# Optimization experiments

Hardware: AMD Instinct MI355X
Metric: run time of the kernel (lower is better)

Reference implementation:

```python
import jax, jax.numpy as jnp
import numpy as np

N = 50000          # nodes
E = 800000         # edges (avg degree 16)
IN = 128           # input feature dim
HID = 64           # hidden dim per head
HEADS = 2          # attention heads (all but last layer)
OUT = 64           # out_dim (last layer, 1 head)
NC = 2             # num_classes
NEG_SLOPE = 0.2    # dgl GATConv leaky_relu slope


def setup_inputs() -> dict:
    key = jax.random.key(0)
    ks = jax.random.split(key, 20)
    rn = lambda k, shape, s=0.05: (jax.random.normal(k, shape, jnp.float32) * s)
    W_IO = HID * HEADS  # 128, width between GAT layers
    return {
        "x": rn(ks[0], (N, IN), 1.0),
        "src": jax.random.randint(ks[1], (E,), 0, N, dtype=jnp.int32),
        "dst": jax.random.randint(ks[2], (E,), 0, N, dtype=jnp.int32),
        # embedding_h: Linear(IN, HID*HEADS)
        "W_emb": rn(ks[3], (IN, W_IO)),
        "b_emb": jnp.zeros((W_IO,), jnp.float32),
        # GAT layer 0: in 128 -> 2 heads x 64
        "W0": rn(ks[4], (W_IO, HEADS * HID)),
        "al0": rn(ks[5], (HEADS, HID)),
        "ar0": rn(ks[6], (HEADS, HID)),
        "b0": jnp.zeros((HEADS * HID,), jnp.float32),
        # GAT layer 1: in 128 -> 2 heads x 64
        "W1": rn(ks[7], (W_IO, HEADS * HID)),
        "al1": rn(ks[8], (HEADS, HID)),
        "ar1": rn(ks[9], (HEADS, HID)),
        "b1": jnp.zeros((HEADS * HID,), jnp.float32),
        # GAT layer 2 (last): in 128 -> 1 head x OUT
        "W2": rn(ks[10], (W_IO, 1 * OUT)),
        "al2": rn(ks[11], (1, OUT)),
        "ar2": rn(ks[12], (1, OUT)),
        "b2": jnp.zeros((OUT,), jnp.float32),
        # edge scorer: Linear(2*OUT, NC)
        "Ws": rn(ks[13], (2 * OUT, NC)),
        "bs": jnp.zeros((NC,), jnp.float32),
    }


def gat_layer(h, src, dst, W, al, ar, b):
    """dgl GATConv + elu (GATLayer with batch_norm=False, residual=False)."""
    heads, out = al.shape
    feat = (h @ W).reshape(-1, heads, out)            # [N,H,D]
    el = jnp.sum(feat * al, axis=-1)                  # [N,H]
    er = jnp.sum(feat * ar, axis=-1)                  # [N,H]
    e = jax.nn.leaky_relu(el[src] + er[dst], NEG_SLOPE)  # [E,H]
    # edge softmax over incoming edges of each dst node
    emax = jax.ops.segment_max(e, dst, num_segments=N)   # [N,H]
    ex = jnp.exp(e - emax[dst])                          # [E,H]
    denom = jax.ops.segment_sum(ex, dst, num_segments=N) # [N,H]
    alpha = ex / jnp.where(denom[dst] > 0, denom[dst], 1.0)
    msg = feat[src] * alpha[:, :, None]                  # [E,H,D]
    rst = jax.ops.segment_sum(msg, dst, num_segments=N)  # [N,H,D]
    rst = rst.reshape(-1, heads * out) + b
    return jax.nn.elu(rst)


def reference(x, W_emb, b_emb, W0, al0, ar0, b0, W1, al1, ar1, b1,
              W2, al2, ar2, b2, Ws, bs, src, dst):
    h = x @ W_emb + b_emb                    # embedding_h (dropout p -> eval/identity)
    h = gat_layer(h, src, dst, W0, al0, ar0, b0)
    h = gat_layer(h, src, dst, W1, al1, ar1, b1)
    h = gat_layer(h, src, dst, W2, al2, ar2, b2)   # [N, OUT]
    # edge scorer on the scored subgraph: concat(src_h, dst_h) -> Linear
    he = jnp.concatenate([h[src], h[dst]], axis=1)  # [E, 2*OUT]
    return he @ Ws + bs                             # [E, NC]
```

## Files before the change

kernel.cpp:

```cpp
#include <hip/hip_runtime.h>
#include <hip/hip_bf16.h>
#include <math.h>


constexpr float SLOPE = 0.2f;

typedef __attribute__((ext_vector_type(8))) short bf16x8;
typedef __attribute__((ext_vector_type(4))) float f32x4;

__device__ __forceinline__ float b2f(unsigned short u) {
  union { unsigned int i; float f; } v;
  v.i = ((unsigned int)u) << 16;
  return v.f;
}
__device__ __forceinline__ unsigned short f2b(float f) {
  unsigned int x = __float_as_uint(f);
  unsigned int r = (x + 0x7fffu + ((x >> 16) & 1u)) >> 16;
  return (unsigned short)r;
}

__global__ void prep_wt(const float* __restrict__ W,
                        unsigned short* __restrict__ Wt, int M) {
  int i = blockIdx.x * 256 + threadIdx.x;
  if (i < 128 * M) {
    int k = i / M, m = i - k * M;
    Wt[m * 128 + k] = f2b(W[i]);
  }
}

template<int M, bool AF32>
__global__ __launch_bounds__(256)
void gemm_mfma(const void* __restrict__ Xv,
               const unsigned short* __restrict__ Wt,
               const float* __restrict__ bias,
               const float* __restrict__ al, const float* __restrict__ ar,
               unsigned short* __restrict__ Yb,
               float* __restrict__ el, float* __restrict__ er, int N) {
  constexpr int NT = M / 16;
  constexpr int H = M / 64;

  const int tid = threadIdx.x;
  const int wave = tid >> 6;
  const int lane = tid & 63;
  const int r = lane & 15;
  const int kg = lane >> 4;
  const int rowbase = blockIdx.x * 64 + wave * 16;
  int grow = rowbase + r;
  int growc = grow < N ? grow : N - 1;

  f32x4 acc[NT];
  #pragma unroll
  for (int t = 0; t < NT; ++t) acc[t] = (f32x4){0.f, 0.f, 0.f, 0.f};

  #pragma unroll
  for (int kk = 0; kk < 4; ++kk) {
    const int k0 = kk * 32 + kg * 8;
    bf16x8 a;
    if constexpr (AF32) {
      const float* X = (const float*)Xv;
      const float4* xp =
          reinterpret_cast<const float4*>(X + (size_t)growc * 128 + k0);
      float4 x0 = xp[0], x1 = xp[1];
      a[0] = (short)f2b(x0.x); a[1] = (short)f2b(x0.y);
      a[2] = (short)f2b(x0.z); a[3] = (short)f2b(x0.w);
      a[4] = (short)f2b(x1.x); a[5] = (short)f2b(x1.y);
      a[6] = (short)f2b(x1.z); a[7] = (short)f2b(x1.w);
    } else {
      const unsigned short* Xb = (const unsigned short*)Xv;
      a = *reinterpret_cast<const bf16x8*>(Xb + (size_t)growc * 128 + k0);
    }
    #pragma unroll
    for (int t = 0; t < NT; ++t) {
      bf16x8 b = *reinterpret_cast<const bf16x8*>(
          Wt + (size_t)(t * 16 + r) * 128 + k0);
      acc[t] = __builtin_amdgcn_mfma_f32_16x16x32_bf16(a, b, acc[t], 0, 0, 0);
    }
  }

  float bv[NT];
  #pragma unroll
  for (int t = 0; t < NT; ++t) bv[t] = bias ? bias[t * 16 + r] : 0.f;
  float alv[NT], arv[NT];
  if (al != nullptr) {
    #pragma unroll
    for (int t = 0; t < NT; ++t) {
      alv[t] = al[t * 16 + r];
      arv[t] = ar[t * 16 + r];
    }
  }

  #pragma unroll
  for (int j = 0; j < 4; ++j) {
    int orow = rowbase + kg * 4 + j;
    bool ok = orow < N;
    if (ok) {
      #pragma unroll
      for (int t = 0; t < NT; ++t)
        Yb[(size_t)orow * M + t * 16 + r] = f2b(acc[t][j] + bv[t]);
    }
    if (al != nullptr) {
      float pl0 = 0.f, pr0 = 0.f, pl1 = 0.f, pr1 = 0.f;
      #pragma unroll
      for (int t = 0; t < 4; ++t) {
        pl0 += acc[t][j] * alv[t];
        pr0 += acc[t][j] * arv[t];
      }
      if constexpr (H == 2) {
        #pragma unroll
        for (int t = 4; t < 8; ++t) {
          pl1 += acc[t][j] * alv[t];
          pr1 += acc[t][j] * arv[t];
        }
      }
      #pragma unroll
      for (int off = 1; off < 16; off <<= 1) {
        pl0 += __shfl_xor(pl0, off);
        pr0 += __shfl_xor(pr0, off);
        if constexpr (H == 2) {
          pl1 += __shfl_xor(pl1, off);
          pr1 += __shfl_xor(pr1, off);
        }
      }
      if (r == 0 && ok) {
        if constexpr (H == 2) {
          el[orow * 2 + 0] = pl0; el[orow * 2 + 1] = pl1;
          er[orow * 2 + 0] = pr0; er[orow * 2 + 1] = pr1;
        } else {
          el[orow] = pl0;
          er[orow] = pr0;
        }
      }
    }
  }
}

__global__ void count_dst(const int* __restrict__ dst, int* __restrict__ cnt,
                          int E) {
  int i = blockIdx.x * blockDim.x + threadIdx.x;
  if (i < E) atomicAdd(&cnt[dst[i]], 1);
}

__global__ void scan1(const int* __restrict__ cnt, int* __restrict__ outv,
                      int* __restrict__ bsum, int n) {
  __shared__ int sm[256];
  int tid = threadIdx.x;
  int base = blockIdx.x * 1024 + tid * 4;
  int pre[4];
  int s = 0;
  #pragma unroll
  for (int j = 0; j < 4; ++j) {
    int idx = base + j;
    int v = (idx < n) ? cnt[idx] : 0;
    pre[j] = s;
    s += v;
  }
  sm[tid] = s;
  __syncthreads();
  for (int off = 1; off < 256; off <<= 1) {
    int a = (tid >= off) ? sm[tid - off] : 0;
    __syncthreads();
    sm[tid] += a;
    __syncthreads();
  }
  int excl = sm[tid] - s;
  #pragma unroll
  for (int j = 0; j < 4; ++j) {
    int idx = base + j;
    if (idx < n) outv[idx] = excl + pre[j];
  }
  if (tid == 255) bsum[blockIdx.x] = sm[255];
}

__global__ void scan2(const int* __restrict__ bsum, int* __restrict__ btop,
                      int nb, int* __restrict__ row_last) {
  if (threadIdx.x == 0 && blockIdx.x == 0) {
    int s = 0;
    for (int i = 0; i < nb; ++i) { btop[i] = s; s += bsum[i]; }
    *row_last = s;
  }
}

__global__ void scan3(int* __restrict__ rp, int* __restrict__ cur,
                      const int* __restrict__ btop, int n) {
  int i = blockIdx.x * blockDim.x + threadIdx.x;
  if (i < n) {
    int v = rp[i] + btop[i >> 10];
    rp[i] = v;
    cur[i] = v;
  }
}

__global__ __launch_bounds__(256)
void scatter_edges(const int* __restrict__ src, const int* __restrict__ dst,
                   int* __restrict__ cur, int* __restrict__ s_csr, int E) {
  int cls = blockIdx.x & 7;
  int grp = blockIdx.x >> 3;
  int nGrp = gridDim.x >> 3;
  for (int base = grp * 256; base < E; base += nGrp * 256) {
    int i = base + threadIdx.x;
    if (i < E) {
      int d = dst[i];
      if (((d >> 4) & 7) == cls) {
        int p = atomicAdd(&cur[d], 1);
        s_csr[p] = src[i];
      }
    }
  }
}

template<int H>
__global__ __launch_bounds__(256)
void edge_prep(const int* __restrict__ s_csr, const float* __restrict__ el,
               const float* __restrict__ er, const int* __restrict__ rp,
               float2* __restrict__ edat, int N, int E) {
  int tid = threadIdx.x;
  int node = blockIdx.x * 16 + (tid >> 4);
  int sl = tid & 15;
  if (node >= N) return;
  int beg = rp[node];
  int end = rp[node + 1];
  if constexpr (H == 2) {
    float2 re = reinterpret_cast<const float2*>(er)[node];
    for (int p = beg + sl; p < end; p += 16) {
      int s = s_csr[p];
      float2 le = reinterpret_cast<const float2*>(el)[s];
      float e0 = le.x + re.x;
      float e1 = le.y + re.y;
      e0 = e0 > 0.f ? e0 : SLOPE * e0;
      e1 = e1 > 0.f ? e1 : SLOPE * e1;
      float sb = __int_as_float(s);
      edat[p] = make_float2(__expf(e0), sb);
      edat[(size_t)E + p] = make_float2(__expf(e1), sb);
    }
  } else {
    float re = er[node];
    for (int p = beg + sl; p < end; p += 16) {
      int s = s_csr[p];
      float ev = el[s] + re;
      ev = ev > 0.f ? ev : SLOPE * ev;
      edat[p] = make_float2(__expf(ev), __int_as_float(s));
    }
  }
}

template<int H, bool SCORE>
__global__ __launch_bounds__(256)
void gat_aggregate(const unsigned short* __restrict__ featb,
                   const float2* __restrict__ edat,
                   const float* __restrict__ bias,
                   const int* __restrict__ row_ptr,
                   unsigned short* __restrict__ houtb,
                   const float* __restrict__ Wsc,
                   float* __restrict__ ps, float* __restrict__ pd,
                   int N, int E) {
  int tid = threadIdx.x;
  int pid = blockIdx.x * 16 + (tid >> 4);
  int sl = tid & 15;
  const int NH = N * H;
  bool live = pid < NH;
  int pc = live ? pid : 0;
  int node, head;
  if constexpr (H == 2) { node = pc >> 1; head = pc & 1; }
  else                  { node = pc;      head = 0; }
  int beg = live ? row_ptr[node] : 0;
  int end = live ? row_ptr[node + 1] : 0;

  const int rowoff = head * 64 + sl * 4;
  const float2* edath = edat + (size_t)head * E;

  float4 acc = make_float4(0.f, 0.f, 0.f, 0.f);
  float den = 0.f;

  for (int p = beg; p < end; p += 8) {
    #pragma unroll
    for (int j = 0; j < 8; ++j) {
      int q = p + j;
      int qc = q < end ? q : end - 1;
      float2 ed = edath[qc];
      float ex = q < end ? ed.x : 0.f;
      int s = __float_as_int(ed.y);
      ushort4 u = *reinterpret_cast<const ushort4*>(
          &featb[(size_t)s * (H * 64) + rowoff]);
      den += ex;
      acc.x += ex * b2f(u.x);
      acc.y += ex * b2f(u.y);
      acc.z += ex * b2f(u.z);
      acc.w += ex * b2f(u.w);
    }
  }

  if (live) {
    float inv = 1.f / (den > 0.f ? den : 1.f);
    float4 bv = reinterpret_cast<const float4*>(bias)[head * 16 + sl];
    float4 r;
    r.x = acc.x * inv + bv.x;
    r.y = acc.y * inv + bv.y;
    r.z = acc.z * inv + bv.z;
    r.w = acc.w * inv + bv.w;
    r.x = r.x > 0.f ? r.x : expm1f(r.x);
    r.y = r.y > 0.f ? r.y : expm1f(r.y);
    r.z = r.z > 0.f ? r.z : expm1f(r.z);
    r.w = r.w > 0.f ? r.w : expm1f(r.w);

    if constexpr (!SCORE) {
      ushort4 o;
      o.x = f2b(r.x); o.y = f2b(r.y); o.z = f2b(r.z); o.w = f2b(r.w);
      *reinterpret_cast<ushort4*>(&houtb[(size_t)pid * 64 + sl * 4]) = o;
    } else {
      float s0 = r.x * Wsc[(4 * sl + 0) * 2] + r.y * Wsc[(4 * sl + 1) * 2] +
                 r.z * Wsc[(4 * sl + 2) * 2] + r.w * Wsc[(4 * sl + 3) * 2];
      float s1 = r.x * Wsc[(4 * sl + 0) * 2 + 1] + r.y * Wsc[(4 * sl + 1) * 2 + 1] +
                 r.z * Wsc[(4 * sl + 2) * 2 + 1] + r.w * Wsc[(4 * sl + 3) * 2 + 1];
      float d0 = r.x * Wsc[(64 + 4 * sl + 0) * 2] + r.y * Wsc[(64 + 4 * sl + 1) * 2] +
                 r.z * Wsc[(64 + 4 * sl + 2) * 2] + r.w * Wsc[(64 + 4 * sl + 3) * 2];
      float d1 = r.x * Wsc[(64 + 4 * sl + 0) * 2 + 1] + r.y * Wsc[(64 + 4 * sl + 1) * 2 + 1] +
                 r.z * Wsc[(64 + 4 * sl + 2) * 2 + 1] + r.w * Wsc[(64 + 4 * sl + 3) * 2 + 1];
      #pragma unroll
      for (int off = 1; off < 16; off <<= 1) {
        s0 += __shfl_xor(s0, off);
        s1 += __shfl_xor(s1, off);
        d0 += __shfl_xor(d0, off);
        d1 += __shfl_xor(d1, off);
      }
      if (sl == 0) {
        ps[node * 2 + 0] = s0;
        ps[node * 2 + 1] = s1;
        pd[node * 2 + 0] = d0;
        pd[node * 2 + 1] = d1;
      }
    }
  }
}

__global__ void score_out(const int* __restrict__ src,
                          const int* __restrict__ dst,
                          const float* __restrict__ ps,
                          const float* __restrict__ pd,
                          const float* __restrict__ bs,
                          float* __restrict__ out, int E) {
  int i = blockIdx.x * blockDim.x + threadIdx.x;
  if (i < E) {
    int s = src[i], d = dst[i];
    float2 a = *reinterpret_cast<const float2*>(ps + (size_t)s * 2);
    float2 b = *reinterpret_cast<const float2*>(pd + (size_t)d * 2);
    float2 o;
    o.x = a.x + b.x + bs[0];
    o.y = a.y + b.y + bs[1];
    *reinterpret_cast<float2*>(out + (size_t)i * 2) = o;
  }
}

extern "C" void kernel_launch(void* const* d_in, const int* in_sizes, int n_in,
                              void* d_out, int out_size, void* d_ws,
                              size_t ws_size, hipStream_t stream) {
  const float* x    = (const float*)d_in[0];
  const int*   src  = (const int*)d_in[1];
  const int*   dst  = (const int*)d_in[2];
  const float* Wemb = (const float*)d_in[3];
  const float* bemb = (const float*)d_in[4];
  const float* W0   = (const float*)d_in[5];
  const float* al0  = (const float*)d_in[6];
  const float* ar0  = (const float*)d_in[7];
  const float* b0   = (const float*)d_in[8];
  const float* W1   = (const float*)d_in[9];
  const float* al1  = (const float*)d_in[10];
  const float* ar1  = (const float*)d_in[11];
  const float* b1   = (const float*)d_in[12];
  const float* W2   = (const float*)d_in[13];
  const float* al2  = (const float*)d_in[14];
  const float* ar2  = (const float*)d_in[15];
  const float* b2   = (const float*)d_in[16];
  const float* Wsc  = (const float*)d_in[17];
  const float* bsc  = (const float*)d_in[18];

  const int N = in_sizes[0] / 128;
  const int E = in_sizes[1];
  float* out = (float*)d_out;

  char* w = (char*)d_ws;
  float2* edat = (float2*)w; w += (size_t)E * 2 * 8;
  unsigned short* Ab = (unsigned short*)w; w += (size_t)N * 128 * 2;
  unsigned short* Bb = (unsigned short*)w; w += (size_t)N * 128 * 2;
  unsigned short* WembT = (unsigned short*)w; w += 128 * 128 * 2;
  unsigned short* W0T   = (unsigned short*)w; w += 128 * 128 * 2;
  unsigned short* W1T   = (unsigned short*)w; w += 128 * 128 * 2;
  unsigned short* W2T   = (unsigned short*)w; w += 128 * 64 * 2;
  float* el  = (float*)w; w += (size_t)N * 2 * 4;
  float* er  = (float*)w; w += (size_t)N * 2 * 4;
  float* ps  = (float*)w; w += (size_t)N * 2 * 4;
  float* pd  = (float*)w; w += (size_t)N * 2 * 4;
  int* s_csr = (int*)w;   w += (size_t)E * 4;
  int* cnt   = (int*)w;   w += (size_t)N * 4;
  int* rp    = (int*)w;   w += (size_t)(N + 4) * 4;
  int* cur   = (int*)w;   w += (size_t)N * 4;
  int* bsum  = (int*)w;   w += 4096;
  int* btop  = (int*)w;   w += 4096;

  prep_wt<<<(128 * 128 + 255) / 256, 256, 0, stream>>>(Wemb, WembT, 128);
  prep_wt<<<(128 * 128 + 255) / 256, 256, 0, stream>>>(W0, W0T, 128);
  prep_wt<<<(128 * 128 + 255) / 256, 256, 0, stream>>>(W1, W1T, 128);
  prep_wt<<<(128 * 64 + 255) / 256, 256, 0, stream>>>(W2, W2T, 64);

  hipMemsetAsync(cnt, 0, (size_t)N * 4, stream);
  count_dst<<<(E + 255) / 256, 256, 0, stream>>>(dst, cnt, E);
  int nb = (N + 1023) / 1024;
  scan1<<<nb, 256, 0, stream>>>(cnt, rp, bsum, N);
  scan2<<<1, 64, 0, stream>>>(bsum, btop, nb, rp + N);
  scan3<<<(N + 255) / 256, 256, 0, stream>>>(rp, cur, btop, N);
  scatter_edges<<<2048, 256, 0, stream>>>(src, dst, cur, s_csr, E);

  const int gb = (N + 63) / 64;
  const int nbk = (N + 15) / 16;
  const int pb2 = (N * 2 + 15) / 16;
  const int pb1 = (N * 1 + 15) / 16;

  gemm_mfma<128, true><<<gb, 256, 0, stream>>>(x, WembT, bemb, nullptr,
                                               nullptr, Ab, nullptr, nullptr,
                                               N);

  gemm_mfma<128, false><<<gb, 256, 0, stream>>>(Ab, W0T, nullptr, al0, ar0,
                                                Bb, el, er, N);
  edge_prep<2><<<nbk, 256, 0, stream>>>(s_csr, el, er, rp, edat, N, E);
  gat_aggregate<2, false><<<pb2, 256, 0, stream>>>(Bb, edat, b0, rp, Ab,
                                                   nullptr, nullptr, nullptr,
                                                   N, E);
  gemm_mfma<128, false><<<gb, 256, 0, stream>>>(Ab, W1T, nullptr, al1, ar1,
                                                Bb, el, er, N);
  edge_prep<2><<<nbk, 256, 0, stream>>>(s_csr, el, er, rp, edat, N, E);
  gat_aggregate<2, false><<<pb2, 256, 0, stream>>>(Bb, edat, b1, rp, Ab,
                                                   nullptr, nullptr, nullptr,
                                                   N, E);
  gemm_mfma<64, false><<<gb, 256, 0, stream>>>(Ab, W2T, nullptr, al2, ar2,
                                               Bb, el, er, N);
  edge_prep<1><<<nbk, 256, 0, stream>>>(s_csr, el, er, rp, edat, N, E);
  gat_aggregate<1, true><<<pb1, 256, 0, stream>>>(Bb, edat, b2, rp, nullptr,
                                                  Wsc, ps, pd, N, E);

  score_out<<<(E + 255) / 256, 256, 0, stream>>>(src, dst, ps, pd, bsc, out, E);
}
```

Baseline: 414.1 us.

## Pad CSR rows to multiples of eight and drop aggregate bounds checks

Each node's CSR row is rounded up to a multiple of eight entries. edge_prep fills the padded slots with zero weight and source index 0, which lets gat_aggregate drop its per-element clamp and mask in the unrolled loop. The change also merges the four weight-transpose launches into one and makes count_dst use the same class-partitioned atomic pattern as scatter_edges. The cost is extra padded edge entries to write and read, a larger workspace, and reliance on cur holding the real row ends after scatter.

```diff
diff --git a/kernel.cpp b/kernel.cpp
--- a/kernel.cpp
+++ b/kernel.cpp
@@ -19,13 +19,23 @@
   return (unsigned short)r;
 }
 
-__global__ void prep_wt(const float* __restrict__ W,
-                        unsigned short* __restrict__ Wt, int M) {
+__global__ void prep_wt_all(const float* __restrict__ Wa,
+                            const float* __restrict__ Wb,
+                            const float* __restrict__ Wc,
+                            const float* __restrict__ Wd,
+                            unsigned short* __restrict__ Ta,
+                            unsigned short* __restrict__ Tb,
+                            unsigned short* __restrict__ Tc,
+                            unsigned short* __restrict__ Td) {
   int i = blockIdx.x * 256 + threadIdx.x;
-  if (i < 128 * M) {
-    int k = i / M, m = i - k * M;
-    Wt[m * 128 + k] = f2b(W[i]);
-  }
+  const float* W; unsigned short* T; int M; int off;
+  if (i < 16384)      { W = Wa; T = Ta; M = 128; off = i; }
+  else if (i < 32768) { W = Wb; T = Tb; M = 128; off = i - 16384; }
+  else if (i < 49152) { W = Wc; T = Tc; M = 128; off = i - 32768; }
+  else if (i < 57344) { W = Wd; T = Td; M = 64;  off = i - 49152; }
+  else return;
+  int k = off / M, m = off - k * M;
+  T[m * 128 + k] = f2b(W[off]);
 }
 
 template<int M, bool AF32>
@@ -134,10 +144,18 @@
   }
 }
 
-__global__ void count_dst(const int* __restrict__ dst, int* __restrict__ cnt,
-                          int E) {
-  int i = blockIdx.x * blockDim.x + threadIdx.x;
-  if (i < E) atomicAdd(&cnt[dst[i]], 1);
+__global__ __launch_bounds__(256)
+void count_dst(const int* __restrict__ dst, int* __restrict__ cnt, int E) {
+  int cls = blockIdx.x & 7;
+  int grp = blockIdx.x >> 3;
+  int nGrp = gridDim.x >> 3;
+  for (int base = grp * 256; base < E; base += nGrp * 256) {
+    int i = base + threadIdx.x;
+    if (i < E) {
+      int d = dst[i];
+      if (((d >> 4) & 7) == cls) atomicAdd(&cnt[d], 1);
+    }
+  }
 }
 
 __global__ void scan1(const int* __restrict__ cnt, int* __restrict__ outv,
@@ -150,7 +168,7 @@
   #pragma unroll
   for (int j = 0; j < 4; ++j) {
     int idx = base + j;
-    int v = (idx < n) ? cnt[idx] : 0;
+    int v = (idx < n) ? ((cnt[idx] + 7) & ~7) : 0;
     pre[j] = s;
     s += v;
   }
@@ -212,16 +230,18 @@
 __global__ __launch_bounds__(256)
 void edge_prep(const int* __restrict__ s_csr, const float* __restrict__ el,
                const float* __restrict__ er, const int* __restrict__ rp,
-               float2* __restrict__ edat, int N, int E) {
+               const int* __restrict__ ends, float2* __restrict__ edat,
+               int N, int EP) {
   int tid = threadIdx.x;
   int node = blockIdx.x * 16 + (tid >> 4);
   int sl = tid & 15;
   if (node >= N) return;
   int beg = rp[node];
-  int end = rp[node + 1];
+  int rend = ends[node];
+  int pend = rp[node + 1];
   if constexpr (H == 2) {
     float2 re = reinterpret_cast<const float2*>(er)[node];
-    for (int p = beg + sl; p < end; p += 16) {
+    for (int p = beg + sl; p < rend; p += 16) {
       int s = s_csr[p];
       float2 le = reinterpret_cast<const float2*>(el)[s];
       float e0 = le.x + re.x;
@@ -230,16 +250,23 @@
       e1 = e1 > 0.f ? e1 : SLOPE * e1;
       float sb = __int_as_float(s);
       edat[p] = make_float2(__expf(e0), sb);
-      edat[(size_t)E + p] = make_float2(__expf(e1), sb);
+      edat[(size_t)EP + p] = make_float2(__expf(e1), sb);
+    }
+    int p2 = rend + sl;
+    if (p2 < pend) {
+      edat[p2] = make_float2(0.f, __int_as_float(0));
+      edat[(size_t)EP + p2] = make_float2(0.f, __int_as_float(0));
     }
   } else {
     float re = er[node];
-    for (int p = beg + sl; p < end; p += 16) {
+    for (int p = beg + sl; p < rend; p += 16) {
       int s = s_csr[p];
       float ev = el[s] + re;
       ev = ev > 0.f ? ev : SLOPE * ev;
       edat[p] = make_float2(__expf(ev), __int_as_float(s));
     }
+    int p2 = rend + sl;
+    if (p2 < pend) edat[p2] = make_float2(0.f, __int_as_float(0));
   }
 }
 
@@ -252,7 +279,7 @@
                    unsigned short* __restrict__ houtb,
                    const float* __restrict__ Wsc,
                    float* __restrict__ ps, float* __restrict__ pd,
-                   int N, int E) {
+                   int N, int EP) {
   int tid = threadIdx.x;
   int pid = blockIdx.x * 16 + (tid >> 4);
   int sl = tid & 15;
@@ -266,7 +293,7 @@
   int end = live ? row_ptr[node + 1] : 0;
 
   const int rowoff = head * 64 + sl * 4;
-  const float2* edath = edat + (size_t)head * E;
+  const float2* edath = edat + (size_t)head * EP;
 
   float4 acc = make_float4(0.f, 0.f, 0.f, 0.f);
   float den = 0.f;
@@ -274,10 +301,8 @@
   for (int p = beg; p < end; p += 8) {
     #pragma unroll
     for (int j = 0; j < 8; ++j) {
-      int q = p + j;
-      int qc = q < end ? q : end - 1;
-      float2 ed = edath[qc];
-      float ex = q < end ? ed.x : 0.f;
+      float2 ed = edath[p + j];
+      float ex = ed.x;
       int s = __float_as_int(ed.y);
       ushort4 u = *reinterpret_cast<const ushort4*>(
           &featb[(size_t)s * (H * 64) + rowoff]);
@@ -376,9 +401,10 @@
   const int N = in_sizes[0] / 128;
   const int E = in_sizes[1];
   float* out = (float*)d_out;
+  const int EP = E + 7 * N + 8;
 
   char* w = (char*)d_ws;
-  float2* edat = (float2*)w; w += (size_t)E * 2 * 8;
+  float2* edat = (float2*)w; w += (size_t)EP * 2 * 8;
   unsigned short* Ab = (unsigned short*)w; w += (size_t)N * 128 * 2;
   unsigned short* Bb = (unsigned short*)w; w += (size_t)N * 128 * 2;
   unsigned short* WembT = (unsigned short*)w; w += 128 * 128 * 2;
@@ -389,20 +415,18 @@
   float* er  = (float*)w; w += (size_t)N * 2 * 4;
   float* ps  = (float*)w; w += (size_t)N * 2 * 4;
   float* pd  = (float*)w; w += (size_t)N * 2 * 4;
-  int* s_csr = (int*)w;   w += (size_t)E * 4;
+  int* s_csr = (int*)w;   w += (size_t)EP * 4;
   int* cnt   = (int*)w;   w += (size_t)N * 4;
   int* rp    = (int*)w;   w += (size_t)(N + 4) * 4;
   int* cur   = (int*)w;   w += (size_t)N * 4;
   int* bsum  = (int*)w;   w += 4096;
   int* btop  = (int*)w;   w += 4096;
 
-  prep_wt<<<(128 * 128 + 255) / 256, 256, 0, stream>>>(Wemb, WembT, 128);
-  prep_wt<<<(128 * 128 + 255) / 256, 256, 0, stream>>>(W0, W0T, 128);
-  prep_wt<<<(128 * 128 + 255) / 256, 256, 0, stream>>>(W1, W1T, 128);
-  prep_wt<<<(128 * 64 + 255) / 256, 256, 0, stream>>>(W2, W2T, 64);
+  prep_wt_all<<<(57344 + 255) / 256, 256, 0, stream>>>(
+      Wemb, W0, W1, W2, WembT, W0T, W1T, W2T);
 
   hipMemsetAsync(cnt, 0, (size_t)N * 4, stream);
-  count_dst<<<(E + 255) / 256, 256, 0, stream>>>(dst, cnt, E);
+  count_dst<<<2048, 256, 0, stream>>>(dst, cnt, E);
   int nb = (N + 1023) / 1024;
   scan1<<<nb, 256, 0, stream>>>(cnt, rp, bsum, N);
   scan2<<<1, 64, 0, stream>>>(bsum, btop, nb, rp + N);
@@ -420,21 +444,21 @@
 
   gemm_mfma<128, false><<<gb, 256, 0, stream>>>(Ab, W0T, nullptr, al0, ar0,
                                                 Bb, el, er, N);
-  edge_prep<2><<<nbk, 256, 0, stream>>>(s_csr, el, er, rp, edat, N, E);
+  edge_prep<2><<<nbk, 256, 0, stream>>>(s_csr, el, er, rp, cur, edat, N, EP);
   gat_aggregate<2, false><<<pb2, 256, 0, stream>>>(Bb, edat, b0, rp, Ab,
                                                    nullptr, nullptr, nullptr,
-                                                   N, E);
+                                                   N, EP);
   gemm_mfma<128, false><<<gb, 256, 0, stream>>>(Ab, W1T, nullptr, al1, ar1,
                                                 Bb, el, er, N);
-  edge_prep<2><<<nbk, 256, 0, stream>>>(s_csr, el, er, rp, edat, N, E);
+  edge_prep<2><<<nbk, 256, 0, stream>>>(s_csr, el, er, rp, cur, edat, N, EP);
   gat_aggregate<2, false><<<pb2, 256, 0, stream>>>(Bb, edat, b1, rp, Ab,
                                                    nullptr, nullptr, nullptr,
-                                                   N, E);
+                                                   N, EP);
   gemm_mfma<64, false><<<gb, 256, 0, stream>>>(Ab, W2T, nullptr, al2, ar2,
                                                Bb, el, er, N);
-  edge_prep<1><<<nbk, 256, 0, stream>>>(s_csr, el, er, rp, edat, N, E);
+  edge_prep<1><<<nbk, 256, 0, stream>>>(s_csr, el, er, rp, cur, edat, N, EP);
   gat_aggregate<1, true><<<pb1, 256, 0, stream>>>(Bb, edat, b2, rp, nullptr,
-                                                  Wsc, ps, pd, N, E);
+                                                  Wsc, ps, pd, N, EP);
 
   score_out<<<(E + 255) / 256, 256, 0, stream>>>(src, dst, ps, pd, bsc, out, E);
 }
```

Result: faster. 393.3 us (median of 2 runs) (-5.0%).
